# Kernel optimization log

Measured on AMD Instinct MI355X. Metric: run time of the kernel, lower is better.

## Reference

```python
import jax, jax.numpy as jnp
import numpy as np

TAU = 0.5  # temperature from init_kwargs


def _semi_loss(h1, h2):
    # GRACE-style InfoNCE: -log( e^{sim(i,i')/tau} / (sum_refl + sum_between - e^{sim(i,i)/tau}) )
    n1 = h1 / jnp.linalg.norm(h1, axis=1, keepdims=True)
    n2 = h2 / jnp.linalg.norm(h2, axis=1, keepdims=True)
    refl = jnp.exp((n1 @ n1.T) / TAU)   # [N, N]
    betw = jnp.exp((n1 @ n2.T) / TAU)   # [N, N]
    denom = refl.sum(axis=1) + betw.sum(axis=1) - jnp.diagonal(refl)
    return -jnp.log(jnp.diagonal(betw) / denom)


def _contrast(h1, h2):
    # forward_v1 with batch_size=0 (batched path is mathematically identical)
    return (0.5 * (_semi_loss(h1, h2) + _semi_loss(h2, h1))).mean()


def _proj(z, Wa, ba, Wb, bb):
    # fc_b(elu(fc_a(z))); torch Linear: y = x @ W.T + b
    return jax.nn.elu(z @ Wa.T + ba) @ Wb.T + bb


def setup_inputs() -> dict:
    key = jax.random.key(0)
    ks = jax.random.split(key, 11)
    N, A, B = 8192, 32, 32
    D = A * B
    s = 1.0 / np.sqrt(D)
    inp = {
        'ta': jax.random.normal(ks[0], (N, A, B), dtype=jnp.float32),
        'tb': jax.random.normal(ks[1], (N, A, B), dtype=jnp.float32),
        'W1': jax.random.uniform(ks[2], (D, D), jnp.float32, -s, s),
        'b1': jax.random.uniform(ks[3], (D,), jnp.float32, -s, s),
        'W2': jax.random.uniform(ks[4], (D, D), jnp.float32, -s, s),
        'b2': jax.random.uniform(ks[5], (D,), jnp.float32, -s, s),
        'W3': jax.random.uniform(ks[6], (D, D), jnp.float32, -s, s),
        'b3': jax.random.uniform(ks[7], (D,), jnp.float32, -s, s),
        'W4': jax.random.uniform(ks[8], (D, D), jnp.float32, -s, s),
        'b4': jax.random.uniform(ks[9], (D,), jnp.float32, -s, s),
        'w_r1': jnp.array([0.5], dtype=jnp.float32),
    }
    return inp


def reference(ta, tb, W1, b1, W2, b2, W3, b3, W4, b4, w_r1):
    N = ta.shape[0]
    # row view: [N, A*B]
    z1 = ta.reshape(N, -1)
    z2 = tb.reshape(N, -1)
    loss_row = _contrast(_proj(z1, W1, b1, W2, b2), _proj(z2, W1, b1, W2, b2))
    # column view: permute(0,2,1) then flatten -> [N, B*A]
    z1c = jnp.transpose(ta, (0, 2, 1)).reshape(N, -1)
    z2c = jnp.transpose(tb, (0, 2, 1)).reshape(N, -1)
    loss_col = _contrast(_proj(z1c, W3, b3, W4, b4), _proj(z2c, W3, b3, W4, b4))
    w_row = jnp.clip(w_r1[0], 0.0, 1.0)
    return w_row * loss_row + (1.0 - w_row) * loss_col
```

## Files before the change

kernel.cpp:

```cpp
#include <hip/hip_runtime.h>
#include <stdint.h>


typedef unsigned short u16;
typedef __attribute__((ext_vector_type(8))) __bf16 bf16x8;
typedef __attribute__((ext_vector_type(4))) float f32x4;

#define NS 8192
#define DD 1024

__device__ __forceinline__ float bf2f(u16 u) {
    union { uint32_t i; float f; } v; v.i = ((uint32_t)u) << 16; return v.f;
}
__device__ __forceinline__ u16 f2bf(float f) {
    union { float f; uint32_t i; } v; v.f = f;
    return (u16)((v.i + 0x7FFFu + ((v.i >> 16) & 1u)) >> 16);
}

__device__ __forceinline__ void gload16(const u16* g, u16* l) {
    __builtin_amdgcn_global_load_lds(
        (__attribute__((address_space(1))) void*)(uintptr_t)(g),
        (__attribute__((address_space(3))) void*)(uintptr_t)(l), 16, 0, 0);
}


__global__ __launch_bounds__(256) void conv_f2bf(const float* __restrict__ src,
                                                 u16* __restrict__ dst) {
    int i = (blockIdx.x * 256 + threadIdx.x) * 4;
    float4 v = *(const float4*)(src + i);
    ushort4 o;
    o.x = f2bf(v.x); o.y = f2bf(v.y); o.z = f2bf(v.z); o.w = f2bf(v.w);
    *(ushort4*)(dst + i) = o;
}

__global__ __launch_bounds__(256) void conv_cat(const float* __restrict__ a,
                                                const float* __restrict__ b,
                                                u16* __restrict__ Z) {
    size_t i = (size_t)(blockIdx.x * 256 + threadIdx.x) * 4;
    const size_t half = (size_t)NS * DD;
    const float* s = (i < half) ? (a + i) : (b + (i - half));
    float4 v = *(const float4*)s;
    ushort4 o;
    o.x = f2bf(v.x); o.y = f2bf(v.y); o.z = f2bf(v.z); o.w = f2bf(v.w);
    *(ushort4*)(Z + i) = o;
}

__global__ __launch_bounds__(256) void conv_col(const float* __restrict__ a,
                                                const float* __restrict__ b,
                                                u16* __restrict__ Z) {
    size_t i = (size_t)(blockIdx.x * 256 + threadIdx.x) * 4;
    const size_t half = (size_t)NS * DD;
    const float* src; size_t o;
    if (i < half) { src = a; o = i; } else { src = b; o = i - half; }
    size_t row = o >> 10;
    int j = (int)(o & 1023);
    int aI = j & 31, bI = j >> 5;
    const float* rp = src + (row << 10);
    ushort4 ov;
    ov.x = f2bf(rp[aI * 32 + bI]);
    ov.y = f2bf(rp[(aI + 1) * 32 + bI]);
    ov.z = f2bf(rp[(aI + 2) * 32 + bI]);
    ov.w = f2bf(rp[(aI + 3) * 32 + bI]);
    *(ushort4*)(Z + i) = ov;
}

template <int MODE>
__global__ __launch_bounds__(256) void gemm_bt(const u16* A, const u16* B,
                                               const float* __restrict__ bias,
                                               u16* __restrict__ out,
                                               float* __restrict__ S) {
    __shared__ alignas(16) u16 As[128 * 32];
    __shared__ alignas(16) u16 Bs[128 * 32];
    const int tid = threadIdx.x;

    int tm, tn;
    if (MODE == 2) {
        int x = blockIdx.x, y = blockIdx.y;
        if (y + x < 128) { tm = y;       tn = y + x; }
        else             { tm = 127 - y; tn = x - 1; }
    } else {
        tm = blockIdx.y; tn = blockIdx.x;
    }
    const size_t tileM = (size_t)tm * 128;
    const size_t tileN = (size_t)tn * 128;

    const u16* gA0 = A + (tileM + (tid >> 2)) * DD + (tid & 3) * 8;
    const u16* gA1 = gA0 + (size_t)64 * DD;
    const u16* gB0 = B + (tileN + (tid >> 2)) * DD + (tid & 3) * 8;
    const u16* gB1 = gB0 + (size_t)64 * DD;
    u16* lA0 = &As[tid * 8]; u16* lA1 = lA0 + 2048;
    u16* lB0 = &Bs[tid * 8]; u16* lB1 = lB0 + 2048;

    const int lane = tid & 63;
    const int wv = tid >> 6;
    const int wr = (wv >> 1) << 6;
    const int wc = (wv & 1) << 6;
    const int lr = lane & 15;
    const int lh = lane >> 4;

    const u16* aBase = &As[(wr + lr) * 32 + lh * 8];
    const u16* bBase = &Bs[(wc + lr) * 32 + lh * 8];

    f32x4 acc[4][4];
#pragma unroll
    for (int i = 0; i < 4; i++)
#pragma unroll
        for (int j = 0; j < 4; j++) acc[i][j] = (f32x4)0.0f;

    for (int k0 = 0; k0 < DD; k0 += 32) {
        gload16(gA0 + k0, lA0);
        gload16(gA1 + k0, lA1);
        gload16(gB0 + k0, lB0);
        gload16(gB1 + k0, lB1);
        __syncthreads();
        bf16x8 af[4], bfr[4];
#pragma unroll
        for (int rt = 0; rt < 4; rt++) af[rt] = *(const bf16x8*)(aBase + rt * 512);
#pragma unroll
        for (int ct = 0; ct < 4; ct++) bfr[ct] = *(const bf16x8*)(bBase + ct * 512);
#pragma unroll
        for (int rt = 0; rt < 4; rt++)
#pragma unroll
            for (int ct = 0; ct < 4; ct++)
                acc[rt][ct] = __builtin_amdgcn_mfma_f32_16x16x32_bf16(
                    af[rt], bfr[ct], acc[rt][ct], 0, 0, 0);
        __syncthreads();
    }

    if (MODE <= 1) {
        float bcol[4];
#pragma unroll
        for (int ct = 0; ct < 4; ct++) bcol[ct] = bias[tileN + wc + ct * 16 + lr];
#pragma unroll
        for (int rt = 0; rt < 4; rt++) {
#pragma unroll
            for (int r = 0; r < 4; r++) {
                size_t row = tileM + wr + rt * 16 + lh * 4 + r;
                u16* orow = out + row * DD + tileN + wc + lr;
#pragma unroll
                for (int ct = 0; ct < 4; ct++) {
                    float v = acc[rt][ct][r] + bcol[ct];
                    if (MODE == 0) v = v > 0.0f ? v : expm1f(v);
                    orow[ct * 16] = f2bf(v);
                }
            }
        }
    } else {
        const bool offdiag = (tm != tn);
        float colsum[4] = {0.f, 0.f, 0.f, 0.f};
#pragma unroll
        for (int rt = 0; rt < 4; rt++) {
#pragma unroll
            for (int r = 0; r < 4; r++) {
                float rs = 0.0f;
#pragma unroll
                for (int ct = 0; ct < 4; ct++) {
                    float e = __expf(2.0f * acc[rt][ct][r]);
                    rs += e;
                    colsum[ct] += e;
                }
                rs += __shfl_xor(rs, 1);
                rs += __shfl_xor(rs, 2);
                rs += __shfl_xor(rs, 4);
                rs += __shfl_xor(rs, 8);
                if (lr == 0) {
                    size_t row = tileM + wr + rt * 16 + lh * 4 + r;
                    atomicAdd(&S[row], rs);
                }
            }
        }
        if (offdiag) {
#pragma unroll
            for (int ct = 0; ct < 4; ct++) {
                float cs = colsum[ct];
                cs += __shfl_xor(cs, 16);
                cs += __shfl_xor(cs, 32);
                if (lh == 0) {
                    size_t col = tileN + wc + ct * 16 + lr;
                    atomicAdd(&S[col], cs);
                }
            }
        }
    }
}

__global__ __launch_bounds__(256) void normalize_kernel(u16* M) {
    __shared__ float red[4];
    const int tid = threadIdx.x;
    u16* row = M + ((size_t)blockIdx.x << 10);
    ushort4 v = ((const ushort4*)row)[tid];
    float x0 = bf2f(v.x), x1 = bf2f(v.y), x2 = bf2f(v.z), x3 = bf2f(v.w);
    float s = x0 * x0 + x1 * x1 + x2 * x2 + x3 * x3;
#pragma unroll
    for (int m = 1; m < 64; m <<= 1) s += __shfl_xor(s, m);
    if ((tid & 63) == 0) red[tid >> 6] = s;
    __syncthreads();
    float inv = rsqrtf(red[0] + red[1] + red[2] + red[3]);
    ushort4 o;
    o.x = f2bf(x0 * inv); o.y = f2bf(x1 * inv);
    o.z = f2bf(x2 * inv); o.w = f2bf(x3 * inv);
    ((ushort4*)row)[tid] = o;
}

__global__ __launch_bounds__(256) void diag_kernel(const u16* M, float* g12) {
    __shared__ float red[4];
    const int tid = threadIdx.x;
    const u16* r1 = M + ((size_t)blockIdx.x << 10);
    const u16* r2 = r1 + ((size_t)NS << 10);
    ushort4 a = ((const ushort4*)r1)[tid];
    ushort4 b = ((const ushort4*)r2)[tid];
    float s = bf2f(a.x) * bf2f(b.x) + bf2f(a.y) * bf2f(b.y) +
              bf2f(a.z) * bf2f(b.z) + bf2f(a.w) * bf2f(b.w);
#pragma unroll
    for (int m = 1; m < 64; m <<= 1) s += __shfl_xor(s, m);
    if ((tid & 63) == 0) red[tid >> 6] = s;
    __syncthreads();
    if (tid == 0) g12[blockIdx.x] = red[0] + red[1] + red[2] + red[3];
}

__global__ __launch_bounds__(256) void final_kernel(const float* Sr, const float* Sc,
                                                    const float* gr, const float* gc,
                                                    const float* w_r1, float* out) {
    __shared__ float red[16];
    const float E2 = 7.389056098930650f;
    float a = 0.f, b = 0.f, c = 0.f, d = 0.f;
    for (int i = threadIdx.x; i < 2 * NS; i += 256) {
        a += logf(Sr[i] - E2);
        b += logf(Sc[i] - E2);
    }
    for (int i = threadIdx.x; i < NS; i += 256) {
        c += gr[i];
        d += gc[i];
    }
#pragma unroll
    for (int m = 1; m < 64; m <<= 1) {
        a += __shfl_xor(a, m); b += __shfl_xor(b, m);
        c += __shfl_xor(c, m); d += __shfl_xor(d, m);
    }
    int w = threadIdx.x >> 6;
    if ((threadIdx.x & 63) == 0) {
        red[w] = a; red[4 + w] = b; red[8 + w] = c; red[12 + w] = d;
    }
    __syncthreads();
    if (threadIdx.x == 0) {
        a = red[0] + red[1] + red[2] + red[3];
        b = red[4] + red[5] + red[6] + red[7];
        c = red[8] + red[9] + red[10] + red[11];
        d = red[12] + red[13] + red[14] + red[15];
        float lr = a / (2.0f * NS) - 2.0f * c / NS;
        float lc = b / (2.0f * NS) - 2.0f * d / NS;
        float w0 = w_r1[0];
        w0 = fminf(fmaxf(w0, 0.0f), 1.0f);
        out[0] = w0 * lr + (1.0f - w0) * lc;
    }
}

extern "C" void kernel_launch(void* const* d_in, const int* in_sizes, int n_in,
                              void* d_out, int out_size, void* d_ws, size_t ws_size,
                              hipStream_t stream) {
    const float* ta = (const float*)d_in[0];
    const float* tb = (const float*)d_in[1];
    const float* W1 = (const float*)d_in[2];
    const float* b1 = (const float*)d_in[3];
    const float* W2 = (const float*)d_in[4];
    const float* b2 = (const float*)d_in[5];
    const float* W3 = (const float*)d_in[6];
    const float* b3 = (const float*)d_in[7];
    const float* W4 = (const float*)d_in[8];
    const float* b4 = (const float*)d_in[9];
    const float* wr = (const float*)d_in[10];
    float* out = (float*)d_out;

    char* p = (char*)d_ws;
    const size_t MAT = (size_t)2 * NS * DD * sizeof(u16);
    u16* Z = (u16*)p;  p += MAT;
    u16* T = (u16*)p;  p += MAT;
    u16* H = (u16*)p;  p += MAT;
    u16* Wb = (u16*)p; p += (size_t)4 * DD * DD * sizeof(u16);
    float* Sr = (float*)p;  p += 2 * NS * sizeof(float);
    float* Sc = (float*)p;  p += 2 * NS * sizeof(float);
    float* gr = (float*)p;  p += NS * sizeof(float);
    float* gc = (float*)p;  p += NS * sizeof(float);

    u16* Wb1 = Wb;
    u16* Wb2 = Wb + (size_t)DD * DD;
    u16* Wb3 = Wb + (size_t)2 * DD * DD;
    u16* Wb4 = Wb + (size_t)3 * DD * DD;

    conv_f2bf<<<1024, 256, 0, stream>>>(W1, Wb1);
    conv_f2bf<<<1024, 256, 0, stream>>>(W2, Wb2);
    conv_f2bf<<<1024, 256, 0, stream>>>(W3, Wb3);
    conv_f2bf<<<1024, 256, 0, stream>>>(W4, Wb4);
    hipMemsetAsync(Sr, 0, 4 * NS * sizeof(float), stream);

    conv_cat<<<16384, 256, 0, stream>>>(ta, tb, Z);
    gemm_bt<0><<<dim3(8, 128), 256, 0, stream>>>(Z, Wb1, b1, T, nullptr);
    gemm_bt<1><<<dim3(8, 128), 256, 0, stream>>>(T, Wb2, b2, H, nullptr);
    normalize_kernel<<<16384, 256, 0, stream>>>(H);
    diag_kernel<<<8192, 256, 0, stream>>>(H, gr);
    gemm_bt<2><<<dim3(129, 64), 256, 0, stream>>>(H, H, nullptr, nullptr, Sr);

    conv_col<<<16384, 256, 0, stream>>>(ta, tb, Z);
    gemm_bt<0><<<dim3(8, 128), 256, 0, stream>>>(Z, Wb3, b3, T, nullptr);
    gemm_bt<1><<<dim3(8, 128), 256, 0, stream>>>(T, Wb4, b4, H, nullptr);
    normalize_kernel<<<16384, 256, 0, stream>>>(H);
    diag_kernel<<<8192, 256, 0, stream>>>(H, gc);
    gemm_bt<2><<<dim3(129, 64), 256, 0, stream>>>(H, H, nullptr, nullptr, Sc);

    final_kernel<<<1, 256, 0, stream>>>(Sr, Sc, gr, gc, wr, out);
}
```

Before: 1.259 ms.

## Replace Gram-matrix GEMM with 256x256-tile kernel using 4-stage LDS pipeline

Adds a dedicated gram256 kernel for the symmetric H·Hᵀ exp-sum. It uses 256x256 tiles with 512 threads, a 4-deep LDS ring buffer fed by direct global-to-LDS loads, XOR-swizzled LDS addressing to cut bank conflicts, and split MFMA phases with barriers and setprio. The larger tiles halve global traffic per FLOP and reduce the number of atomics per element, while the pipeline hides load latency. In exchange it uses 128KB of LDS per block, which limits occupancy to one block per CU, and it adds hand-tuned waitcnt logic that is fragile.

```diff
diff --git a/kernel.cpp b/kernel.cpp
--- a/kernel.cpp
+++ b/kernel.cpp
@@ -67,20 +67,12 @@
 template <int MODE>
 __global__ __launch_bounds__(256) void gemm_bt(const u16* A, const u16* B,
                                                const float* __restrict__ bias,
-                                               u16* __restrict__ out,
-                                               float* __restrict__ S) {
+                                               u16* __restrict__ out) {
     __shared__ alignas(16) u16 As[128 * 32];
     __shared__ alignas(16) u16 Bs[128 * 32];
     const int tid = threadIdx.x;
 
-    int tm, tn;
-    if (MODE == 2) {
-        int x = blockIdx.x, y = blockIdx.y;
-        if (y + x < 128) { tm = y;       tn = y + x; }
-        else             { tm = 127 - y; tn = x - 1; }
-    } else {
-        tm = blockIdx.y; tn = blockIdx.x;
-    }
+    const int tm = blockIdx.y, tn = blockIdx.x;
     const size_t tileM = (size_t)tm * 128;
     const size_t tileN = (size_t)tn * 128;
 
@@ -127,58 +119,160 @@
         __syncthreads();
     }
 
-    if (MODE <= 1) {
-        float bcol[4];
-#pragma unroll
-        for (int ct = 0; ct < 4; ct++) bcol[ct] = bias[tileN + wc + ct * 16 + lr];
-#pragma unroll
-        for (int rt = 0; rt < 4; rt++) {
-#pragma unroll
-            for (int r = 0; r < 4; r++) {
-                size_t row = tileM + wr + rt * 16 + lh * 4 + r;
-                u16* orow = out + row * DD + tileN + wc + lr;
-#pragma unroll
-                for (int ct = 0; ct < 4; ct++) {
-                    float v = acc[rt][ct][r] + bcol[ct];
-                    if (MODE == 0) v = v > 0.0f ? v : expm1f(v);
-                    orow[ct * 16] = f2bf(v);
-                }
+    float bcol[4];
+#pragma unroll
+    for (int ct = 0; ct < 4; ct++) bcol[ct] = bias[tileN + wc + ct * 16 + lr];
+#pragma unroll
+    for (int rt = 0; rt < 4; rt++) {
+#pragma unroll
+        for (int r = 0; r < 4; r++) {
+            size_t row = tileM + wr + rt * 16 + lh * 4 + r;
+            u16* orow = out + row * DD + tileN + wc + lr;
+#pragma unroll
+            for (int ct = 0; ct < 4; ct++) {
+                float v = acc[rt][ct][r] + bcol[ct];
+                if (MODE == 0) v = v > 0.0f ? v : expm1f(v);
+                orow[ct * 16] = f2bf(v);
             }
         }
-    } else {
-        const bool offdiag = (tm != tn);
-        float colsum[4] = {0.f, 0.f, 0.f, 0.f};
-#pragma unroll
-        for (int rt = 0; rt < 4; rt++) {
-#pragma unroll
-            for (int r = 0; r < 4; r++) {
-                float rs = 0.0f;
-#pragma unroll
-                for (int ct = 0; ct < 4; ct++) {
-                    float e = __expf(2.0f * acc[rt][ct][r]);
-                    rs += e;
-                    colsum[ct] += e;
-                }
-                rs += __shfl_xor(rs, 1);
-                rs += __shfl_xor(rs, 2);
-                rs += __shfl_xor(rs, 4);
-                rs += __shfl_xor(rs, 8);
-                if (lr == 0) {
-                    size_t row = tileM + wr + rt * 16 + lh * 4 + r;
-                    atomicAdd(&S[row], rs);
-                }
+    }
+}
+
+__global__ __launch_bounds__(512) void gram256(const u16* __restrict__ H,
+                                               float* __restrict__ S) {
+    __shared__ alignas(16) u16 LA[4][256 * 32];
+    __shared__ alignas(16) u16 LB[4][256 * 32];
+    const int tid = threadIdx.x;
+
+    int x = blockIdx.x, y = blockIdx.y;
+    int tm, tn;
+    if (y + x < 64) { tm = y;      tn = y + x; }
+    else            { tm = 63 - y; tn = x - 1; }
+
+    const size_t rowA = (size_t)tm * 256;
+    const size_t rowB = (size_t)tn * 256;
+
+    const int r_lo = tid >> 2;
+    const int s_st = tid & 3;
+    const int csw  = (s_st ^ (r_lo & 3)) * 8;
+    const u16* gA0 = H + (rowA + r_lo) * DD + csw;
+    const u16* gA1 = H + (rowA + 128 + r_lo) * DD + csw;
+    const u16* gB0 = H + (rowB + r_lo) * DD + csw;
+    const u16* gB1 = H + (rowB + 128 + r_lo) * DD + csw;
+    const int ldst = tid * 8;
+
+    const int lane = tid & 63;
+    const int wv = tid >> 6;
+    const int wr = (wv >> 2) * 128;
+    const int wc = (wv & 3) * 64;
+    const int lr = lane & 15;
+    const int lh = lane >> 4;
+    const int sw = lh ^ (lr & 3);
+    const int aoff = (wr + lr) * 32 + sw * 8;
+    const int boff = (wc + lr) * 32 + sw * 8;
+
+    f32x4 acc[8][4];
+#pragma unroll
+    for (int i = 0; i < 8; ++i)
+#pragma unroll
+        for (int j = 0; j < 4; ++j) acc[i][j] = (f32x4)0.0f;
+
+#pragma unroll
+    for (int t = 0; t < 3; ++t) {
+        const int k0 = t * 32;
+        gload16(gA0 + k0, &LA[t][0] + ldst);
+        gload16(gA1 + k0, &LA[t][4096] + ldst);
+        gload16(gB0 + k0, &LB[t][0] + ldst);
+        gload16(gB1 + k0, &LB[t][4096] + ldst);
+    }
+    asm volatile("s_waitcnt vmcnt(8)" ::: "memory");
+    __builtin_amdgcn_s_barrier();
+
+    for (int t = 0; t < 32; ++t) {
+        const int buf = t & 3;
+        const u16* la = &LA[buf][0];
+        const u16* lb = &LB[buf][0];
+        const int nbuf = (t + 3) & 3;
+        const int k0n = (t + 3) * 32;
+        bf16x8 aF[4], bF[4];
+
+#pragma unroll
+        for (int i = 0; i < 4; ++i) aF[i] = *(const bf16x8*)(la + aoff + i * 512);
+#pragma unroll
+        for (int i = 0; i < 4; ++i) bF[i] = *(const bf16x8*)(lb + boff + i * 512);
+        if (t < 29) {
+            gload16(gA0 + k0n, &LA[nbuf][0] + ldst);
+            gload16(gA1 + k0n, &LA[nbuf][4096] + ldst);
+        }
+        asm volatile("" ::: "memory");
+        __builtin_amdgcn_s_barrier();
+        asm volatile("s_waitcnt lgkmcnt(0)" ::: "memory");
+        __builtin_amdgcn_sched_barrier(0);
+        __builtin_amdgcn_s_setprio(1);
+#pragma unroll
+        for (int mi = 0; mi < 4; ++mi)
+#pragma unroll
+            for (int ni = 0; ni < 4; ++ni)
+                acc[mi][ni] = __builtin_amdgcn_mfma_f32_16x16x32_bf16(
+                    aF[mi], bF[ni], acc[mi][ni], 0, 0, 0);
+        __builtin_amdgcn_s_setprio(0);
+        __builtin_amdgcn_s_barrier();
+
+#pragma unroll
+        for (int i = 0; i < 4; ++i) aF[i] = *(const bf16x8*)(la + aoff + 2048 + i * 512);
+        if (t < 29) {
+            gload16(gB0 + k0n, &LB[nbuf][0] + ldst);
+            gload16(gB1 + k0n, &LB[nbuf][4096] + ldst);
+        }
+        if (t < 29)       asm volatile("s_waitcnt vmcnt(8)" ::: "memory");
+        else if (t == 29) asm volatile("s_waitcnt vmcnt(4)" ::: "memory");
+        else if (t == 30) asm volatile("s_waitcnt vmcnt(0)" ::: "memory");
+        __builtin_amdgcn_s_barrier();
+        asm volatile("s_waitcnt lgkmcnt(0)" ::: "memory");
+        __builtin_amdgcn_sched_barrier(0);
+        __builtin_amdgcn_s_setprio(1);
+#pragma unroll
+        for (int mi = 0; mi < 4; ++mi)
+#pragma unroll
+            for (int ni = 0; ni < 4; ++ni)
+                acc[4 + mi][ni] = __builtin_amdgcn_mfma_f32_16x16x32_bf16(
+                    aF[mi], bF[ni], acc[4 + mi][ni], 0, 0, 0);
+        __builtin_amdgcn_s_setprio(0);
+        __builtin_amdgcn_s_barrier();
+    }
+
+    const bool offdiag = (tm != tn);
+    float colsum[4] = {0.f, 0.f, 0.f, 0.f};
+#pragma unroll
+    for (int q = 0; q < 8; ++q) {
+#pragma unroll
+        for (int r = 0; r < 4; ++r) {
+            float rs = 0.0f;
+#pragma unroll
+            for (int ni = 0; ni < 4; ++ni) {
+                float e = __expf(2.0f * acc[q][ni][r]);
+                rs += e;
+                colsum[ni] += e;
+            }
+            rs += __shfl_xor(rs, 1);
+            rs += __shfl_xor(rs, 2);
+            rs += __shfl_xor(rs, 4);
+            rs += __shfl_xor(rs, 8);
+            if (lr == 0) {
+                size_t row = rowA + wr + q * 16 + lh * 4 + r;
+                atomicAdd(&S[row], rs);
             }
         }
-        if (offdiag) {
-#pragma unroll
-            for (int ct = 0; ct < 4; ct++) {
-                float cs = colsum[ct];
-                cs += __shfl_xor(cs, 16);
-                cs += __shfl_xor(cs, 32);
-                if (lh == 0) {
-                    size_t col = tileN + wc + ct * 16 + lr;
-                    atomicAdd(&S[col], cs);
-                }
+    }
+    if (offdiag) {
+#pragma unroll
+        for (int ni = 0; ni < 4; ++ni) {
+            float cs = colsum[ni];
+            cs += __shfl_xor(cs, 16);
+            cs += __shfl_xor(cs, 32);
+            if (lh == 0) {
+                size_t col = rowB + wc + ni * 16 + lr;
+                atomicAdd(&S[col], cs);
             }
         }
     }
@@ -294,18 +388,18 @@
     hipMemsetAsync(Sr, 0, 4 * NS * sizeof(float), stream);
 
     conv_cat<<<16384, 256, 0, stream>>>(ta, tb, Z);
-    gemm_bt<0><<<dim3(8, 128), 256, 0, stream>>>(Z, Wb1, b1, T, nullptr);
-    gemm_bt<1><<<dim3(8, 128), 256, 0, stream>>>(T, Wb2, b2, H, nullptr);
+    gemm_bt<0><<<dim3(8, 128), 256, 0, stream>>>(Z, Wb1, b1, T);
+    gemm_bt<1><<<dim3(8, 128), 256, 0, stream>>>(T, Wb2, b2, H);
     normalize_kernel<<<16384, 256, 0, stream>>>(H);
     diag_kernel<<<8192, 256, 0, stream>>>(H, gr);
-    gemm_bt<2><<<dim3(129, 64), 256, 0, stream>>>(H, H, nullptr, nullptr, Sr);
+    gram256<<<dim3(65, 32), 512, 0, stream>>>(H, Sr);
 
     conv_col<<<16384, 256, 0, stream>>>(ta, tb, Z);
-    gemm_bt<0><<<dim3(8, 128), 256, 0, stream>>>(Z, Wb3, b3, T, nullptr);
-    gemm_bt<1><<<dim3(8, 128), 256, 0, stream>>>(T, Wb4, b4, H, nullptr);
+    gemm_bt<0><<<dim3(8, 128), 256, 0, stream>>>(Z, Wb3, b3, T);
+    gemm_bt<1><<<dim3(8, 128), 256, 0, stream>>>(T, Wb4, b4, H);
     normalize_kernel<<<16384, 256, 0, stream>>>(H);
     diag_kernel<<<8192, 256, 0, stream>>>(H, gc);
-    gemm_bt<2><<<dim3(129, 64), 256, 0, stream>>>(H, H, nullptr, nullptr, Sc);
+    gram256<<<dim3(65, 32), 512, 0, stream>>>(H, Sc);
 
     final_kernel<<<1, 256, 0, stream>>>(Sr, Sc, gr, gc, wr, out);
 }
```

New measurement: 1.273 ms. No clear change (+1.1%).
